# Kernel tuning notes

Hardware: AMD Instinct MI355X
Metric: run time of the kernel (lower is better)

## Reference

```python
import jax, jax.numpy as jnp
import numpy as np

B, S, D, H, HD, K, FF, G, E = 2, 2048, 512, 8, 64, 31, 2048, 4, 2
EPS = 1e-6


def _layer_norm(x, scale, bias):
    m = jnp.mean(x, axis=-1, keepdims=True)
    v = jnp.var(x, axis=-1, keepdims=True)
    return (x - m) * jax.lax.rsqrt(v + EPS) * scale + bias


def _forward(x, group_ids, p):
    (ln1_s, ln1_b, ck, cb, ln2_s, ln2_b,
     wq, bq, wk, bk, wv, bv, wo, bo, w1, b1, w2, b2) = p
    # ---- conv sublayer: LN -> Conv1d(SAME) -> gelu -> residual ----
    r = x
    h = _layer_norm(x, ln1_s, ln1_b)
    h = jax.lax.conv_general_dilated(h, ck, (1,), 'SAME',
                                     dimension_numbers=('NWC', 'WIO', 'NWC')) + cb
    x = jax.nn.gelu(h) + r
    # ---- self-attention sublayer: LN -> MHA -> residual ----
    r = x
    h = _layer_norm(x, ln2_s, ln2_b)
    q = jnp.einsum('bsd,dhk->bshk', h, wq) + bq   # [B,S,H,HD]
    k = jnp.einsum('bsd,dhk->bshk', h, wk) + bk
    v = jnp.einsum('bsd,dhk->bshk', h, wv) + bv
    scale = jnp.asarray(1.0 / np.sqrt(HD), h.dtype)
    att = jax.nn.softmax(jnp.einsum('bqhk,bshk->bhqs', q, k) * scale, axis=-1)
    o = jnp.einsum('bhqs,bshk->bqhk', att, v)
    x = jnp.einsum('bqhk,hkd->bqd', o, wo) + bo + r
    # ---- MoE sublayer: group tokens -> per-group experts -> mean -> combine ----
    r = x
    xf = x.reshape(-1, D)            # [N, D]
    gid = group_ids.reshape(-1)      # [N]
    # Each token routed by group_id gets the mean over that group's E experts.
    hid = jax.nn.gelu(jnp.einsum('nd,gedf->genf', xf, w1) + b1[:, :, None, :])  # [G,E,N,FF]
    ye = jnp.einsum('genf,gefd->gend', hid, w2) + b2[:, :, None, :]             # [G,E,N,D]
    yg = ye.mean(axis=1)                                                        # [G,N,D]
    sel = yg[gid, jnp.arange(gid.shape[0])]                                     # [N,D] combine by group id
    return sel.reshape(B, S, D) + r


def setup_inputs() -> dict:
    key = jax.random.key(0)
    ks = jax.random.split(key, 12)
    std = 0.02
    f32 = jnp.float32
    return {
        'x': jax.random.normal(ks[0], (B, S, D), f32),
        'group_ids': jax.random.randint(ks[1], (B, S), 0, G, jnp.int32),
        'ln1_scale': jnp.ones((D,), f32), 'ln1_bias': jnp.zeros((D,), f32),
        'conv_kernel': jax.random.normal(ks[2], (K, D, D), f32) * std,
        'conv_bias': jnp.zeros((D,), f32),
        'ln2_scale': jnp.ones((D,), f32), 'ln2_bias': jnp.zeros((D,), f32),
        'wq': jax.random.normal(ks[3], (D, H, HD), f32) * std, 'bq': jnp.zeros((H, HD), f32),
        'wk': jax.random.normal(ks[4], (D, H, HD), f32) * std, 'bk': jnp.zeros((H, HD), f32),
        'wv': jax.random.normal(ks[5], (D, H, HD), f32) * std, 'bv': jnp.zeros((H, HD), f32),
        'wo': jax.random.normal(ks[6], (H, HD, D), f32) * std, 'bo': jnp.zeros((D,), f32),
        'w1': jax.random.normal(ks[7], (G, E, D, FF), f32) * std, 'b1': jnp.zeros((G, E, FF), f32),
        'w2': jax.random.normal(ks[8], (G, E, FF, D), f32) * std, 'b2': jnp.zeros((G, E, D), f32),
    }


def reference(x, group_ids, ln1_scale, ln1_bias, conv_kernel, conv_bias,
              ln2_scale, ln2_bias, wq, bq, wk, bk, wv, bv, wo, bo,
              w1, b1, w2, b2):
    p = (ln1_scale, ln1_bias, conv_kernel, conv_bias, ln2_scale, ln2_bias,
         wq, bq, wk, bk, wv, bv, wo, bo, w1, b1, w2, b2)
    return _forward(x, group_ids, p)
```

## Files before the change

kernel.cpp:

```cpp
#include <hip/hip_runtime.h>
#include <hip/hip_bf16.h>
#include <math.h>
#include <stdint.h>

namespace {

constexpr int B_ = 2, S_ = 2048, D_ = 512, H_ = 8, HD_ = 64, K_ = 31,
              FF_ = 2048, G_ = 4, E_ = 2;
constexpr int N_ = B_ * S_;
constexpr int SP_ = S_ + 30;
constexpr float EPS_ = 1e-6f;
constexpr int PADCAP_ = 4608;

typedef __bf16 bf16x8 __attribute__((ext_vector_type(8)));
typedef unsigned short u16x8 __attribute__((ext_vector_type(8)));
typedef unsigned short u16x4 __attribute__((ext_vector_type(4)));
typedef float f32x4 __attribute__((ext_vector_type(4)));

__device__ __forceinline__ uint16_t f2bf(float f) {
  union { float f; uint32_t u; } v; v.f = f;
  uint32_t r = v.u + 0x7FFFu + ((v.u >> 16) & 1u);
  return (uint16_t)(r >> 16);
}
__device__ __forceinline__ float bf2f(uint16_t u) {
  union { uint32_t u; float f; } v; v.u = (uint32_t)u << 16;
  return v.f;
}

__device__ __forceinline__ float gelu_f(float x) {
  const float c = 0.7978845608028654f;
  return 0.5f * x * (1.0f + tanhf(c * (x + 0.044715f * x * x * x)));
}

#define GLOAD_LDS16(gsrc, ldst)                                              \
  __builtin_amdgcn_global_load_lds(                                          \
      (const __attribute__((address_space(1))) void*)(gsrc),                 \
      (__attribute__((address_space(3))) void*)(ldst), 16, 0, 0)

#define VMCNT(n) asm volatile("s_waitcnt vmcnt(" #n ")" ::: "memory")
#define MEMBAR asm volatile("" ::: "memory")
#define BARRIER __builtin_amdgcn_s_barrier()
#define PRIO1 __builtin_amdgcn_s_setprio(1)
#define PRIO0 __builtin_amdgcn_s_setprio(0)

__device__ __forceinline__ void kstep_swz(const char* As, const char* Bs,
                                          int wr, int wc, int l15, int g,
                                          f32x4 acc[4][4]) {
#pragma unroll
  for (int ks = 0; ks < 2; ++ks) {
    int co = (((ks << 2) | g) ^ (l15 & 7)) << 4;
    bf16x8 a[4], b[4];
#pragma unroll
    for (int m = 0; m < 4; ++m)
      a[m] = *(const bf16x8*)(As + (wr * 64 + m * 16 + l15) * 128 + co);
#pragma unroll
    for (int n = 0; n < 4; ++n)
      b[n] = *(const bf16x8*)(Bs + (wc * 64 + n * 16 + l15) * 128 + co);
    PRIO1;
#pragma unroll
    for (int m = 0; m < 4; ++m)
#pragma unroll
      for (int n = 0; n < 4; ++n)
        acc[m][n] = __builtin_amdgcn_mfma_f32_16x16x32_bf16(a[m], b[n], acc[m][n], 0, 0, 0);
    PRIO0;
  }
}

template <int NK>
__device__ __forceinline__ void gemm_k_dbuf64(const uint16_t* Ab, int lda,
                                              const uint16_t* Bb, int ldb,
                                              int t, int wr, int wc, int l15, int g,
                                              uint16_t (*As)[8192], uint16_t (*Bs)[8192],
                                              f32x4 acc[4][4]) {
  int r8 = t >> 3, clog = (t & 7) ^ (r8 & 7);
  int ubase = (t & ~63) * 8;
  auto stage = [&](int k0, int buf) {
#pragma unroll
    for (int pi = 0; pi < 4; ++pi) {
      int row = pi * 32 + r8;
      GLOAD_LDS16(Ab + (size_t)row * lda + k0 + clog * 8, As[buf] + pi * 2048 + ubase);
      GLOAD_LDS16(Bb + (size_t)row * ldb + k0 + clog * 8, Bs[buf] + pi * 2048 + ubase);
    }
  };
  stage(0, 0);
  int cur = 0;
  for (int ki = 0; ki < NK; ++ki) {
    if (ki + 1 < NK) {
      stage((ki + 1) * 64, cur ^ 1);
      VMCNT(8);
    } else {
      VMCNT(0);
    }
    BARRIER; MEMBAR;
    kstep_swz((const char*)As[cur], (const char*)Bs[cur], wr, wc, l15, g, acc);
    MEMBAR; BARRIER;
    cur ^= 1;
  }
}

__global__ __launch_bounds__(256) void prep_kernel(
    const float* __restrict__ ck, const float* __restrict__ wq,
    const float* __restrict__ wk, const float* __restrict__ wv,
    const float* __restrict__ wo, const float* __restrict__ w1,
    const float* __restrict__ w2, uint16_t* __restrict__ ckT,
    uint16_t* __restrict__ wqkvT, uint16_t* __restrict__ woT,
    uint16_t* __restrict__ w1T, uint16_t* __restrict__ w2T,
    uint16_t* __restrict__ Hpad, uint16_t* __restrict__ x2bf,
    const float* __restrict__ x, const float* __restrict__ ln1s,
    const float* __restrict__ ln1b, const int* __restrict__ gid,
    int* __restrict__ list, int* __restrict__ poff) {
  int bi = blockIdx.x, t = threadIdx.x;
  if (bi >= 25406) {
    int row = bi - 25406;
    const float* xr = x + (size_t)row * D_;
    float v0 = xr[t], v1 = xr[t + 256];
    float s = v0 + v1, sq = v0 * v0 + v1 * v1;
    for (int o = 32; o > 0; o >>= 1) {
      s += __shfl_down(s, o);
      sq += __shfl_down(sq, o);
    }
    __shared__ float sm[8];
    __shared__ float mr[2];
    int lane = t & 63, wid = t >> 6;
    if (lane == 0) { sm[wid] = s; sm[wid + 4] = sq; }
    __syncthreads();
    if (t == 0) {
      float ts = sm[0] + sm[1] + sm[2] + sm[3];
      float tq = sm[4] + sm[5] + sm[6] + sm[7];
      float m = ts / D_;
      mr[0] = m;
      mr[1] = rsqrtf(tq / D_ - m * m + EPS_);
    }
    __syncthreads();
    float m = mr[0], rs = mr[1];
    size_t drow = (size_t)(row >> 11) * SP_ + 15 + (row & 2047);
    uint16_t* orow = Hpad + drow * D_;
    orow[t] = f2bf((v0 - m) * rs * ln1s[t] + ln1b[t]);
    orow[t + 256] = f2bf((v1 - m) * rs * ln1s[t + 256] + ln1b[t + 256]);
    return;
  }
  if (bi == 25405) {
    __shared__ int cnt[G_], cur[G_];
    if (t < G_) cnt[t] = 0;
    __syncthreads();
    for (int i = t; i < N_; i += 256) atomicAdd(&cnt[gid[i]], 1);
    __syncthreads();
    if (t == 0) {
      int off = 0;
      for (int g = 0; g < G_; ++g) {
        poff[g] = off;
        cur[g] = off;
        off += (cnt[g] + 127) & ~127;
      }
      poff[G_] = off;
    }
    __syncthreads();
    for (int i = t; i < PADCAP_; i += 256) list[i] = N_;
    __syncthreads();
    for (int i = t; i < N_; i += 256) {
      int p = atomicAdd(&cur[gid[i]], 1);
      list[p] = i;
    }
    return;
  }
  if (bi >= 25344) {
    int j4 = bi - 25344;
    uint16_t* dst;
    if (j4 < 60) {
      int b = j4 / 30, j = j4 % 30;
      int row = b * SP_ + (j < 15 ? j : 2048 + j);
      dst = Hpad + (size_t)row * D_;
    } else {
      dst = x2bf + (size_t)N_ * D_;
    }
    dst[t] = 0;
    dst[t + 256] = 0;
    return;
  }
  const float* src;
  uint16_t* dst;
  int R, C, r0, c0;
  if (bi < 7936) {
    int z = bi >> 8, tile = bi & 255;
    R = 512; C = 512;
    c0 = (tile & 15) * 32; r0 = (tile >> 4) * 32;
    src = ck + (size_t)z * 262144; dst = ckT + (size_t)z * 262144;
  } else if (bi < 8960) {
    int idx = bi - 7936, mat = idx >> 8, tile = idx & 255;
    R = 512; C = 512;
    c0 = (tile & 15) * 32; r0 = (tile >> 4) * 32;
    src = mat == 0 ? wq : (mat == 1 ? wk : (mat == 2 ? wv : wo));
    dst = mat == 3 ? woT : wqkvT + (size_t)mat * 262144;
  } else if (bi < 17152) {
    int idx = bi - 8960, z = idx >> 10, tile = idx & 1023;
    R = 512; C = 2048;
    c0 = (tile & 63) * 32; r0 = (tile >> 6) * 32;
    src = w1 + (size_t)z * 1048576; dst = w1T + (size_t)z * 1048576;
  } else {
    int idx = bi - 17152, z = idx >> 10, tile = idx & 1023;
    R = 2048; C = 512;
    c0 = (tile & 15) * 32; r0 = (tile >> 4) * 32;
    src = w2 + (size_t)z * 1048576; dst = w2T + (size_t)z * 1048576;
  }
  __shared__ float tile[32][33];
  int tc = t & 31, tr = t >> 5;
#pragma unroll
  for (int i = 0; i < 4; ++i) {
    int r = tr + i * 8;
    tile[r][tc] = src[(size_t)(r0 + r) * C + c0 + tc];
  }
  __syncthreads();
#pragma unroll
  for (int i = 0; i < 4; ++i) {
    int rr = tr + i * 8;
    dst[(size_t)(c0 + rr) * R + r0 + tc] = f2bf(tile[tc][rr]);
  }
}

__global__ __launch_bounds__(512) void conv_mfma_kernel(
    const uint16_t* __restrict__ Hpad, const uint16_t* __restrict__ ckT,
    uint16_t* __restrict__ Pout) {
  __shared__ __align__(16) uint16_t As[2][20480];
  __shared__ __align__(16) uint16_t Bs[2][16384];
  int bid = blockIdx.x;
  int ks = bid & 7, tmn = bid >> 3, tm = tmn & 15, tn = tmn >> 4;
  int t = threadIdx.x;
  int w = t >> 6, l = t & 63, l15 = l & 15, g = l >> 4;
  int wr = w >> 2, wc = w & 3;
  int row0 = tm * 256, b = row0 >> 11, s0 = row0 & 2047;
  int kb = ks * 4, ntap = (ks == 7) ? 3 : 4;
  const uint16_t* Abase = Hpad + (size_t)(b * SP_ + s0 + kb) * D_;
  int r8 = t >> 3, clog = (t & 7) ^ (r8 & 7);
  int ubase = (t & ~63) * 8;
  f32x4 acc[8][4] = {};

  auto stageA = [&](int d0, int buf) {
#pragma unroll
    for (int pi = 0; pi < 5; ++pi)
      GLOAD_LDS16(Abase + (size_t)(pi * 64 + r8) * D_ + d0 + clog * 8,
                  As[buf] + pi * 4096 + ubase);
  };
  auto stageB = [&](int k, int d0, int buf) {
    const uint16_t* Bk = ckT + (size_t)k * D_ * D_ + (size_t)(tn * 256) * D_;
#pragma unroll
    for (int pi = 0; pi < 4; ++pi)
      GLOAD_LDS16(Bk + (size_t)(pi * 64 + r8) * D_ + d0 + clog * 8,
                  Bs[buf] + pi * 4096 + ubase);
  };

  stageA(0, 0);
  stageB(kb, 0, 0);
  int acur = 0, bcur = 0;
  for (int di = 0; di < 8; ++di) {
    int d0 = di * 64;
    for (int i = 0; i < ntap; ++i) {
      if (i + 1 < ntap) {
        stageB(kb + i + 1, d0, bcur ^ 1);
        VMCNT(4);
      } else if (di + 1 < 8) {
        stageA(d0 + 64, acur ^ 1);
        stageB(kb, d0 + 64, bcur ^ 1);
        VMCNT(9);
      } else {
        VMCNT(0);
      }
      BARRIER; MEMBAR;
      const char* Ac = (const char*)As[acur];
      const char* Bc = (const char*)Bs[bcur];
#pragma unroll
      for (int kk = 0; kk < 2; ++kk) {
        int cA = (((kk << 2) | g) ^ ((i + l15) & 7)) << 4;
        int cB = (((kk << 2) | g) ^ (l15 & 7)) << 4;
        bf16x8 a[8], bb[4];
#pragma unroll
        for (int m = 0; m < 8; ++m)
          a[m] = *(const bf16x8*)(Ac + (i + wr * 128 + m * 16 + l15) * 128 + cA);
#pragma unroll
        for (int n = 0; n < 4; ++n)
          bb[n] = *(const bf16x8*)(Bc + (wc * 64 + n * 16 + l15) * 128 + cB);
        PRIO1;
#pragma unroll
        for (int m = 0; m < 8; ++m)
#pragma unroll
          for (int n = 0; n < 4; ++n)
            acc[m][n] = __builtin_amdgcn_mfma_f32_16x16x32_bf16(a[m], bb[n], acc[m][n], 0, 0, 0);
        PRIO0;
      }
      MEMBAR; BARRIER;
      bcur ^= 1;
    }
    acur ^= 1;
  }
  uint16_t* P = Pout + (size_t)ks * N_ * D_;
#pragma unroll
  for (int m = 0; m < 8; ++m) {
    int r = row0 + wr * 128 + m * 16 + g * 4;
#pragma unroll
    for (int n = 0; n < 4; ++n) {
      int c = tn * 256 + wc * 64 + n * 16 + l15;
#pragma unroll
      for (int j = 0; j < 4; ++j)
        P[(size_t)(r + j) * D_ + c] = f2bf(acc[m][n][j]);
    }
  }
}

__global__ __launch_bounds__(256) void epi_ln_kernel(
    const uint16_t* __restrict__ P, const float* __restrict__ cb,
    const float* __restrict__ xres, const float* __restrict__ ln2s,
    const float* __restrict__ ln2b, float* __restrict__ x1,
    uint16_t* __restrict__ ln2bf) {
  int t = threadIdx.x;
  int row = blockIdx.x * 4 + (t >> 6);
  int l = t & 63, d0 = l * 8;
  size_t base = (size_t)row * D_ + d0;
  float v[8] = {};
#pragma unroll
  for (int q = 0; q < 8; ++q) {
    u16x8 pv = *(const u16x8*)(P + (size_t)q * N_ * D_ + base);
#pragma unroll
    for (int j = 0; j < 8; ++j) v[j] += bf2f(pv[j]);
  }
  float s = 0.f, sq = 0.f;
#pragma unroll
  for (int j = 0; j < 8; ++j) {
    float xv = xres[base + j];
    float vv = gelu_f(v[j] + cb[d0 + j]) + xv;
    v[j] = vv;
    s += vv;
    sq += vv * vv;
  }
  float4 o0 = {v[0], v[1], v[2], v[3]};
  float4 o1 = {v[4], v[5], v[6], v[7]};
  *(float4*)(x1 + base) = o0;
  *(float4*)(x1 + base + 4) = o1;
  for (int o = 1; o < 64; o <<= 1) {
    s += __shfl_xor(s, o);
    sq += __shfl_xor(sq, o);
  }
  float m = s / D_;
  float rs = rsqrtf(sq / D_ - m * m + EPS_);
  u16x8 ob;
#pragma unroll
  for (int j = 0; j < 8; ++j)
    ob[j] = f2bf((v[j] - m) * rs * ln2s[d0 + j] + ln2b[d0 + j]);
  *(u16x8*)(ln2bf + base) = ob;
}

__global__ __launch_bounds__(256) void gemm_qkv_kernel(
    const uint16_t* __restrict__ A, const uint16_t* __restrict__ BT,
    const float* __restrict__ bq, const float* __restrict__ bk,
    const float* __restrict__ bv, uint16_t* __restrict__ Qb,
    uint16_t* __restrict__ Kb, uint16_t* __restrict__ VT) {
  __shared__ __align__(16) uint16_t As[2][8192], Bs[2][8192];
  int tm = blockIdx.x, tn = blockIdx.y;
  int t = threadIdx.x;
  int w = t >> 6, l = t & 63, l15 = l & 15, g = l >> 4;
  int wr = w >> 1, wc = w & 1;
  int row0 = tm * 128;
  f32x4 acc[4][4] = {};
  gemm_k_dbuf64<8>(A + (size_t)row0 * D_, D_, BT + (size_t)(tn * 128) * D_, D_,
                   t, wr, wc, l15, g, As, Bs, acc);
  int sel = tn >> 2, col0 = (tn & 3) * 128;
  if (sel < 2) {
    uint16_t* dst = sel == 0 ? Qb : Kb;
    const float* bias = sel == 0 ? bq : bk;
    float scl = sel == 0 ? 0.125f : 1.0f;
#pragma unroll
    for (int m = 0; m < 4; ++m) {
      int r = row0 + wr * 64 + m * 16 + g * 4;
#pragma unroll
      for (int n = 0; n < 4; ++n) {
        int c = col0 + wc * 64 + n * 16 + l15;
#pragma unroll
        for (int j = 0; j < 4; ++j)
          dst[(size_t)(r + j) * D_ + c] = f2bf((acc[m][n][j] + bias[c]) * scl);
      }
    }
  } else {
#pragma unroll
    for (int m = 0; m < 4; ++m) {
      int tb = row0 + wr * 64 + m * 16 + g * 4;
      int b = tb >> 11, s = tb & 2047;
#pragma unroll
      for (int n = 0; n < 4; ++n) {
        int c = col0 + wc * 64 + n * 16 + l15;
        int hh = c >> 6, d = c & 63;
        u16x4 pack;
#pragma unroll
        for (int j = 0; j < 4; ++j) pack[j] = f2bf(acc[m][n][j] + bv[c]);
        *(u16x4*)(VT + ((size_t)((b * H_ + hh) * HD_ + d) * S_ + s)) = pack;
      }
    }
  }
}

__global__ __launch_bounds__(256) void gemm_wo_kernel(
    const uint16_t* __restrict__ A, const uint16_t* __restrict__ BT,
    const float* __restrict__ bo, const float* __restrict__ res,
    float* __restrict__ out, uint16_t* __restrict__ x2bf) {
  __shared__ __align__(16) uint16_t As[2][8192], Bs[2][8192];
  int tm = blockIdx.x, tn = blockIdx.y;
  int t = threadIdx.x;
  int w = t >> 6, l = t & 63, l15 = l & 15, g = l >> 4;
  int wr = w >> 1, wc = w & 1;
  int row0 = tm * 128;
  f32x4 acc[4][4] = {};
  gemm_k_dbuf64<8>(A + (size_t)row0 * D_, D_, BT + (size_t)(tn * 128) * D_, D_,
                   t, wr, wc, l15, g, As, Bs, acc);
#pragma unroll
  for (int m = 0; m < 4; ++m) {
    int r = row0 + wr * 64 + m * 16 + g * 4;
#pragma unroll
    for (int n = 0; n < 4; ++n) {
      int c = tn * 128 + wc * 64 + n * 16 + l15;
#pragma unroll
      for (int j = 0; j < 4; ++j) {
        float v = acc[m][n][j] + bo[c] + res[(size_t)(r + j) * D_ + c];
        out[(size_t)(r + j) * D_ + c] = v;
        x2bf[(size_t)(r + j) * D_ + c] = f2bf(v);
      }
    }
  }
}

__global__ __launch_bounds__(512) void attn_mfma_kernel(
    const uint16_t* __restrict__ Qbf, const uint16_t* __restrict__ Kbf,
    const uint16_t* __restrict__ VT, uint16_t* __restrict__ obf) {
  __shared__ __align__(16) uint16_t Ks[2][4096];
  __shared__ __align__(16) uint16_t Vt[2][4096];
  __shared__ __align__(16) uint16_t Plds[8192];
  int qt = blockIdx.x, h = blockIdx.y, b = blockIdx.z;
  int t = threadIdx.x, w = t >> 6, l = t & 63;
  int l15 = l & 15, g = l >> 4;
  int qbase = b * S_ + qt * 128;
  bf16x8 qb_[2];
  {
    const uint16_t* qp = Qbf + (size_t)(qbase + w * 16 + l15) * D_ + h * HD_;
#pragma unroll
    for (int ks = 0; ks < 2; ++ks)
      qb_[ks] = *(const bf16x8*)(qp + ks * 32 + g * 8);
  }
  const uint16_t* Kbase = Kbf + (size_t)(b * S_) * D_ + h * HD_;
  const uint16_t* Vbase = VT + (size_t)((b * H_ + h) * HD_) * S_;
  int r0 = t >> 3, slot = t & 7;
  int sb0 = (slot * 16) ^ ((r0 & 7) << 4);
  int ldst = (t & ~63) * 16;

  auto stage_kv = [&](int kt, int buf) {
    const uint16_t* Kp = Kbase + (size_t)(kt * 64) * D_;
    const uint16_t* Vp = Vbase + kt * 64;
    GLOAD_LDS16((const char*)(Kp + (size_t)r0 * D_) + sb0, (char*)Ks[buf] + ldst);
    GLOAD_LDS16((const char*)(Vp + (size_t)r0 * S_) + sb0, (char*)Vt[buf] + ldst);
  };

  f32x4 acc_o[4] = {};
  float m_run = -INFINITY, l_run = 0.f;
  char* Pw = (char*)Plds + w * 2048;

  stage_kv(0, 0);
  int cur = 0;
  for (int kt = 0; kt < S_ / 64; ++kt) {
    if (kt + 1 < S_ / 64) {
      stage_kv(kt + 1, cur ^ 1);
      VMCNT(2);
    } else {
      VMCNT(0);
    }
    BARRIER; MEMBAR;
    const char* KsC = (const char*)Ks[cur];
    const char* VtC = (const char*)Vt[cur];
    f32x4 accs[4] = {};
#pragma unroll
    for (int ks = 0; ks < 2; ++ks) {
#pragma unroll
      for (int m = 0; m < 4; ++m) {
        int row = m * 16 + l15;
        bf16x8 kf = *(const bf16x8*)(KsC +
                        (row * 128 + ((ks * 64 + g * 16) ^ ((row & 7) << 4))));
        PRIO1;
        accs[m] = __builtin_amdgcn_mfma_f32_16x16x32_bf16(kf, qb_[ks], accs[m], 0, 0, 0);
        PRIO0;
      }
    }
    float mx = accs[0][0];
#pragma unroll
    for (int m = 0; m < 4; ++m)
#pragma unroll
      for (int j = 0; j < 4; ++j) mx = fmaxf(mx, accs[m][j]);
    mx = fmaxf(mx, __shfl_xor(mx, 16));
    mx = fmaxf(mx, __shfl_xor(mx, 32));
    float mnew = fmaxf(m_run, mx);
    float corr = __expf(m_run - mnew);
    m_run = mnew;
    float sum = 0.f;
#pragma unroll
    for (int m = 0; m < 4; ++m) {
      float p0 = __expf(accs[m][0] - mnew);
      float p1 = __expf(accs[m][1] - mnew);
      float p2 = __expf(accs[m][2] - mnew);
      float p3 = __expf(accs[m][3] - mnew);
      sum += (p0 + p1) + (p2 + p3);
      uint2 pk;
      pk.x = (uint32_t)f2bf(p0) | ((uint32_t)f2bf(p1) << 16);
      pk.y = (uint32_t)f2bf(p2) | ((uint32_t)f2bf(p3) << 16);
      *(uint2*)(Pw + (l15 * 128 + ((m * 32 + g * 8) ^ ((l15 & 7) << 4)))) = pk;
    }
    sum += __shfl_xor(sum, 16);
    sum += __shfl_xor(sum, 32);
    l_run = l_run * corr + sum;
    float cj[4];
#pragma unroll
    for (int j = 0; j < 4; ++j) cj[j] = __shfl(corr, g * 4 + j);
#pragma unroll
    for (int n = 0; n < 4; ++n)
#pragma unroll
      for (int j = 0; j < 4; ++j) acc_o[n][j] *= cj[j];
#pragma unroll
    for (int ks = 0; ks < 2; ++ks) {
      bf16x8 pa = *(const bf16x8*)(Pw +
                      (l15 * 128 + ((ks * 64 + g * 16) ^ ((l15 & 7) << 4))));
#pragma unroll
      for (int n = 0; n < 4; ++n) {
        int d = n * 16 + l15;
        bf16x8 vb = *(const bf16x8*)(VtC +
                        (d * 128 + ((ks * 64 + g * 16) ^ ((d & 7) << 4))));
        PRIO1;
        acc_o[n] = __builtin_amdgcn_mfma_f32_16x16x32_bf16(pa, vb, acc_o[n], 0, 0, 0);
        PRIO0;
      }
    }
    MEMBAR; BARRIER;
    cur ^= 1;
  }
#pragma unroll
  for (int j = 0; j < 4; ++j) {
    float lr = __shfl(l_run, g * 4 + j);
    float inv = 1.f / lr;
    uint16_t* op = obf + (size_t)(qbase + w * 16 + g * 4 + j) * D_ + h * HD_;
#pragma unroll
    for (int n = 0; n < 4; ++n)
      op[n * 16 + l15] = f2bf(acc_o[n][j] * inv);
  }
}

__global__ __launch_bounds__(256) void ff1_mfma_kernel(
    const uint16_t* __restrict__ X, const uint16_t* __restrict__ w1T,
    const float* __restrict__ b1, const int* __restrict__ list,
    const int* __restrict__ poff, uint16_t* __restrict__ hid) {
  __shared__ __align__(16) uint16_t As[2][8192], Bs[2][8192];
  int tm = blockIdx.x, tn = blockIdx.y, e = blockIdx.z;
  int slot0 = tm * 128;
  if (slot0 >= poff[G_]) return;
  int g_ = 0;
#pragma unroll
  for (int gg = 1; gg < G_; ++gg) g_ += (slot0 >= poff[gg]);
  int t = threadIdx.x;
  int w = t >> 6, l = t & 63, l15 = l & 15, g = l >> 4;
  int wr = w >> 1, wc = w & 1;
  int r8 = t >> 3, clog = (t & 7) ^ (r8 & 7);
  int ubase = (t & ~63) * 8;
  int tok[4];
#pragma unroll
  for (int pi = 0; pi < 4; ++pi) tok[pi] = list[slot0 + pi * 32 + r8];
  const uint16_t* Bb = w1T + ((size_t)(g_ * E_ + e) * FF_ + tn * 128) * D_;
  f32x4 acc[4][4] = {};
  auto stage = [&](int k0, int buf) {
#pragma unroll
    for (int pi = 0; pi < 4; ++pi) {
      GLOAD_LDS16(X + (size_t)tok[pi] * D_ + k0 + clog * 8, As[buf] + pi * 2048 + ubase);
      GLOAD_LDS16(Bb + (size_t)(pi * 32 + r8) * D_ + k0 + clog * 8,
                  Bs[buf] + pi * 2048 + ubase);
    }
  };
  stage(0, 0);
  int cur = 0;
  for (int ki = 0; ki < 8; ++ki) {
    if (ki + 1 < 8) {
      stage((ki + 1) * 64, cur ^ 1);
      VMCNT(8);
    } else {
      VMCNT(0);
    }
    BARRIER; MEMBAR;
    kstep_swz((const char*)As[cur], (const char*)Bs[cur], wr, wc, l15, g, acc);
    MEMBAR; BARRIER;
    cur ^= 1;
  }
  const float* bias = b1 + (size_t)(g_ * E_ + e) * FF_;
  uint16_t* hidE = hid + (size_t)e * PADCAP_ * FF_;
#pragma unroll
  for (int m = 0; m < 4; ++m) {
    int r = slot0 + wr * 64 + m * 16 + g * 4;
#pragma unroll
    for (int n = 0; n < 4; ++n) {
      int c = tn * 128 + wc * 64 + n * 16 + l15;
#pragma unroll
      for (int j = 0; j < 4; ++j)
        hidE[(size_t)(r + j) * FF_ + c] = f2bf(gelu_f(acc[m][n][j] + bias[c]));
    }
  }
}

__global__ __launch_bounds__(256) void ff2_mfma_kernel(
    const uint16_t* __restrict__ hid, const uint16_t* __restrict__ w2T,
    const float* __restrict__ b2, const int* __restrict__ list,
    const int* __restrict__ poff, float* __restrict__ out) {
  __shared__ __align__(16) uint16_t As[2][8192], Bs[2][8192];
  int tm = blockIdx.x, tn = blockIdx.y, z = blockIdx.z;
  int e = z >> 1, kh = z & 1;
  int slot0 = tm * 128;
  if (slot0 >= poff[G_]) return;
  int g_ = 0;
#pragma unroll
  for (int gg = 1; gg < G_; ++gg) g_ += (slot0 >= poff[gg]);
  int t = threadIdx.x;
  int w = t >> 6, l = t & 63, l15 = l & 15, g = l >> 4;
  int wr = w >> 1, wc = w & 1;
  f32x4 acc[4][4] = {};
  const uint16_t* Ab = hid + ((size_t)e * PADCAP_ + slot0) * FF_ + kh * 1024;
  const uint16_t* Bb = w2T + (size_t)(g_ * E_ + e) * D_ * FF_ +
                       (size_t)(tn * 128) * FF_ + kh * 1024;
  gemm_k_dbuf64<16>(Ab, FF_, Bb, FF_, t, wr, wc, l15, g, As, Bs, acc);
  const float* be = b2 + (size_t)(g_ * E_ + e) * D_;
  float bs = (kh == 0) ? 0.5f : 0.f;
#pragma unroll
  for (int m = 0; m < 4; ++m) {
    int rbase = slot0 + wr * 64 + m * 16 + g * 4;
#pragma unroll
    for (int j = 0; j < 4; ++j) {
      int tok = list[rbase + j];
      if (tok >= N_) continue;
#pragma unroll
      for (int n = 0; n < 4; ++n) {
        int c = tn * 128 + wc * 64 + n * 16 + l15;
        atomicAdd(&out[(size_t)tok * D_ + c], 0.5f * acc[m][n][j] + bs * be[c]);
      }
    }
  }
}

}

extern "C" void kernel_launch(void* const* d_in, const int* in_sizes, int n_in,
                              void* d_out, int out_size, void* d_ws, size_t ws_size,
                              hipStream_t stream) {
  const float* x = (const float*)d_in[0];
  const int* gid = (const int*)d_in[1];
  const float* ln1s = (const float*)d_in[2];
  const float* ln1b = (const float*)d_in[3];
  const float* ck = (const float*)d_in[4];
  const float* cb = (const float*)d_in[5];
  const float* ln2s = (const float*)d_in[6];
  const float* ln2b = (const float*)d_in[7];
  const float* wq = (const float*)d_in[8];
  const float* bq = (const float*)d_in[9];
  const float* wk = (const float*)d_in[10];
  const float* bk = (const float*)d_in[11];
  const float* wv = (const float*)d_in[12];
  const float* bv = (const float*)d_in[13];
  const float* wo = (const float*)d_in[14];
  const float* bo = (const float*)d_in[15];
  const float* w1 = (const float*)d_in[16];
  const float* b1 = (const float*)d_in[17];
  const float* w2 = (const float*)d_in[18];
  const float* b2 = (const float*)d_in[19];
  float* out = (float*)d_out;

  char* ws = (char*)d_ws;
  char* A = ws;
  uint16_t* P = (uint16_t*)A;
  uint16_t* ln2bf = (uint16_t*)(A + (32ull << 20));
  uint16_t* Qbf = (uint16_t*)A;
  uint16_t* Kbf = (uint16_t*)(A + (4ull << 20));
  uint16_t* VT = (uint16_t*)(A + (8ull << 20));
  uint16_t* obf = (uint16_t*)(A + (12ull << 20));
  uint16_t* hidbf = (uint16_t*)A;

  float* x1 = (float*)(ws + (38ull << 20));
  uint16_t* Hpad = (uint16_t*)(ws + (46ull << 20));
  uint16_t* ckT = (uint16_t*)(ws + (51ull << 20));
  uint16_t* wqkvT = (uint16_t*)(ws + (67ull << 20));
  uint16_t* woT = (uint16_t*)(ws + (69ull << 20));
  uint16_t* w1T = (uint16_t*)(ws + (70ull << 20));
  uint16_t* w2T = (uint16_t*)(ws + (86ull << 20));
  uint16_t* x2bf = (uint16_t*)(ws + (102ull << 20));
  int* list = (int*)(ws + (107ull << 20));
  int* poff = list + PADCAP_;

  prep_kernel<<<29502, 256, 0, stream>>>(ck, wq, wk, wv, wo, w1, w2,
                                         ckT, wqkvT, woT, w1T, w2T, Hpad, x2bf,
                                         x, ln1s, ln1b, gid, list, poff);

  conv_mfma_kernel<<<256, 512, 0, stream>>>(Hpad, ckT, P);
  epi_ln_kernel<<<1024, 256, 0, stream>>>(P, cb, x, ln2s, ln2b, x1, ln2bf);

  gemm_qkv_kernel<<<dim3(32, 12), 256, 0, stream>>>(ln2bf, wqkvT, bq, bk, bv, Qbf, Kbf, VT);
  attn_mfma_kernel<<<dim3(S_ / 128, H_, B_), 512, 0, stream>>>(Qbf, Kbf, VT, obf);
  gemm_wo_kernel<<<dim3(32, 4), 256, 0, stream>>>(obf, woT, bo, x1, out, x2bf);

  ff1_mfma_kernel<<<dim3(36, 16, 2), 256, 0, stream>>>(x2bf, w1T, b1, list, poff, hidbf);
  ff2_mfma_kernel<<<dim3(36, 4, 4), 256, 0, stream>>>(hidbf, w2T, b2, list, poff, out);
}
```

Before: 341.8 us.

## Replace split-K FF2 GEMM with full-K 64-row tiles

The FF2 expert GEMM used to split K into two halves across blocks (128x128 tiles), and both halves atomically added into the output. It now uses 64x128 output tiles that each run the full 2048-long K loop with an inline double-buffered LDS pipeline. The grid stays at the same block count, but atomic traffic to the output is halved. In exchange each block runs a longer serial K loop, and reuse of the B tile is lower per loaded A row.

```diff
diff --git a/kernel.cpp b/kernel.cpp
--- a/kernel.cpp
+++ b/kernel.cpp
@@ -606,10 +606,10 @@
     const uint16_t* __restrict__ hid, const uint16_t* __restrict__ w2T,
     const float* __restrict__ b2, const int* __restrict__ list,
     const int* __restrict__ poff, float* __restrict__ out) {
-  __shared__ __align__(16) uint16_t As[2][8192], Bs[2][8192];
-  int tm = blockIdx.x, tn = blockIdx.y, z = blockIdx.z;
-  int e = z >> 1, kh = z & 1;
-  int slot0 = tm * 128;
+  __shared__ __align__(16) uint16_t As[2][4096];
+  __shared__ __align__(16) uint16_t Bs[2][8192];
+  int tm = blockIdx.x, tn = blockIdx.y, e = blockIdx.z;
+  int slot0 = tm * 64;
   if (slot0 >= poff[G_]) return;
   int g_ = 0;
 #pragma unroll
@@ -617,16 +617,58 @@
   int t = threadIdx.x;
   int w = t >> 6, l = t & 63, l15 = l & 15, g = l >> 4;
   int wr = w >> 1, wc = w & 1;
-  f32x4 acc[4][4] = {};
-  const uint16_t* Ab = hid + ((size_t)e * PADCAP_ + slot0) * FF_ + kh * 1024;
-  const uint16_t* Bb = w2T + (size_t)(g_ * E_ + e) * D_ * FF_ +
-                       (size_t)(tn * 128) * FF_ + kh * 1024;
-  gemm_k_dbuf64<16>(Ab, FF_, Bb, FF_, t, wr, wc, l15, g, As, Bs, acc);
+  int r8 = t >> 3, clog = (t & 7) ^ (r8 & 7);
+  int ubase = (t & ~63) * 8;
+  const uint16_t* Ab = hid + ((size_t)e * PADCAP_ + slot0) * FF_;
+  const uint16_t* Bb = w2T + (size_t)(g_ * E_ + e) * D_ * FF_ + (size_t)(tn * 128) * FF_;
+  f32x4 acc[2][4] = {};
+  auto stage = [&](int k0, int buf) {
+#pragma unroll
+    for (int pi = 0; pi < 2; ++pi)
+      GLOAD_LDS16(Ab + (size_t)(pi * 32 + r8) * FF_ + k0 + clog * 8,
+                  As[buf] + pi * 2048 + ubase);
+#pragma unroll
+    for (int pi = 0; pi < 4; ++pi)
+      GLOAD_LDS16(Bb + (size_t)(pi * 32 + r8) * FF_ + k0 + clog * 8,
+                  Bs[buf] + pi * 2048 + ubase);
+  };
+  stage(0, 0);
+  int cur = 0;
+  for (int ki = 0; ki < 32; ++ki) {
+    if (ki + 1 < 32) {
+      stage((ki + 1) * 64, cur ^ 1);
+      VMCNT(6);
+    } else {
+      VMCNT(0);
+    }
+    BARRIER; MEMBAR;
+    const char* Ac = (const char*)As[cur];
+    const char* Bc = (const char*)Bs[cur];
+#pragma unroll
+    for (int ks = 0; ks < 2; ++ks) {
+      int co = (((ks << 2) | g) ^ (l15 & 7)) << 4;
+      bf16x8 a[2], b[4];
+#pragma unroll
+      for (int m = 0; m < 2; ++m)
+        a[m] = *(const bf16x8*)(Ac + (wr * 32 + m * 16 + l15) * 128 + co);
+#pragma unroll
+      for (int n = 0; n < 4; ++n)
+        b[n] = *(const bf16x8*)(Bc + (wc * 64 + n * 16 + l15) * 128 + co);
+      PRIO1;
+#pragma unroll
+      for (int m = 0; m < 2; ++m)
+#pragma unroll
+        for (int n = 0; n < 4; ++n)
+          acc[m][n] = __builtin_amdgcn_mfma_f32_16x16x32_bf16(a[m], b[n], acc[m][n], 0, 0, 0);
+      PRIO0;
+    }
+    MEMBAR; BARRIER;
+    cur ^= 1;
+  }
   const float* be = b2 + (size_t)(g_ * E_ + e) * D_;
-  float bs = (kh == 0) ? 0.5f : 0.f;
-#pragma unroll
-  for (int m = 0; m < 4; ++m) {
-    int rbase = slot0 + wr * 64 + m * 16 + g * 4;
+#pragma unroll
+  for (int m = 0; m < 2; ++m) {
+    int rbase = slot0 + wr * 32 + m * 16 + g * 4;
 #pragma unroll
     for (int j = 0; j < 4; ++j) {
       int tok = list[rbase + j];
@@ -634,7 +676,7 @@
 #pragma unroll
       for (int n = 0; n < 4; ++n) {
         int c = tn * 128 + wc * 64 + n * 16 + l15;
-        atomicAdd(&out[(size_t)tok * D_ + c], 0.5f * acc[m][n][j] + bs * be[c]);
+        atomicAdd(&out[(size_t)tok * D_ + c], 0.5f * (acc[m][n][j] + be[c]));
       }
     }
   }
@@ -700,5 +742,5 @@
   gemm_wo_kernel<<<dim3(32, 4), 256, 0, stream>>>(obf, woT, bo, x1, out, x2bf);
 
   ff1_mfma_kernel<<<dim3(36, 16, 2), 256, 0, stream>>>(x2bf, w1T, b1, list, poff, hidbf);
-  ff2_mfma_kernel<<<dim3(36, 4, 4), 256, 0, stream>>>(hidbf, w2T, b2, list, poff, out);
-}
+  ff2_mfma_kernel<<<dim3(72, 4, 2), 256, 0, stream>>>(hidbf, w2T, b2, list, poff, out);
+}
```

Result: faster. 291.0 us (-14.9%).
